# Kernel tuning notes

Measured on AMD Instinct MI355X. Metric: run time of the kernel, lower is better.

## Reference

```python
import jax, jax.numpy as jnp
import numpy as np
from jax import lax

MIN_R = 0.01
RADIUS = 0.8
NSAMPLE = 32
PRED_NSAMPLE = 16
TEMPERATURE = 1.0
DIV_COEF = 10.0
GRID3 = 64  # grid_size**3, grid_size=4
EPS = 1e-5


def _ball_query(q, xyz, radius, nsample):
    """q (M,3), xyz (N,3), radius scalar or (M,). Returns idx (M,nsample) int32, empty (M,) bool.
    Mirrors stack ball_query CUDA op: first-found neighbors within radius, padded with first index."""
    N = xyz.shape[0]
    d2 = jnp.sum((q[:, None, :] - xyz[None, :, :]) ** 2, axis=-1)  # (M,N)
    r = jnp.broadcast_to(jnp.asarray(radius, d2.dtype), (q.shape[0],))[:, None]
    valid = d2 < r * r
    score = jnp.where(valid, -jnp.arange(N, dtype=jnp.int32), -(N + 1))
    vals, _ = lax.top_k(score, nsample)  # largest score == smallest valid index
    idx = -vals
    pad = idx == (N + 1)
    idx = jnp.where(pad, idx[:, :1], idx)  # pad with first found neighbor
    empty = pad[:, 0]                       # no neighbor at all
    idx = jnp.where(empty[:, None], 0, idx)
    return idx, empty


def _group(q, xyz, feats, idx, empty):
    """QueryAndGroup gather: relative xyz concat point features; zero empty queries.
    Returns (M, nsample, 3+C)."""
    g_xyz = xyz[idx] - q[:, None, :]
    g = jnp.concatenate([g_xyz, feats[idx]], axis=-1)
    return jnp.where(empty[:, None, None], jnp.zeros((), g.dtype), g)


def _mlp(x, params):
    """Shared 1x1 Conv2d + BatchNorm2d(training stats) + ReLU stack. x: (B,M,S,C)."""
    for W, g, b in params:
        x = jnp.einsum('bmsc,cd->bmsd', x, W)
        mu = x.mean(axis=(0, 1, 2))
        var = x.var(axis=(0, 1, 2))
        x = (x - mu) * lax.rsqrt(var + EPS) * g + b
        x = jax.nn.relu(x)
    return x


def setup_inputs() -> dict:
    key = jax.random.key(0)
    ks = jax.random.split(key, 16)
    B, N, C, R, Croi = 2, 8192, 32, 64, 128
    scene = jnp.array([10.0, 10.0, 4.0], jnp.float32)
    xyz = jax.random.uniform(ks[0], (B, N, 3), jnp.float32) * scene
    features = jax.random.normal(ks[1], (B, N, C), jnp.float32)
    rois = jax.random.uniform(ks[2], (B, R, GRID3, 3), jnp.float32) * scene
    roi_features = jax.random.normal(ks[3], (B, R, Croi), jnp.float32)

    def kaiming(k, fi, fo):
        return jax.random.normal(k, (fi, fo), jnp.float32) * np.float32(np.sqrt(2.0 / fi))

    return {
        'xyz': xyz, 'features': features, 'rois': rois, 'roi_features': roi_features,
        'temperature_decay': jnp.ones((1,), jnp.float32),
        # predict mlp: [32+3, 32, 32]
        'pw0': kaiming(ks[4], 35, 32), 'pg0': jnp.ones(32), 'pb0': jnp.zeros(32),
        'pw1': kaiming(ks[5], 32, 32), 'pg1': jnp.ones(32), 'pb1': jnp.zeros(32),
        # feat mlp: [32+3, 64, 64]
        'fw0': kaiming(ks[6], 35, 64), 'fg0': jnp.ones(64), 'fb0': jnp.zeros(64),
        'fw1': kaiming(ks[7], 64, 64), 'fg1': jnp.ones(64), 'fb1': jnp.zeros(64),
        # predict fc: [32*64 + 128, 1]
        'fcw': kaiming(ks[8], 2176, 1), 'fcb': jnp.zeros(1),
    }


def reference(xyz, features, rois, roi_features, temperature_decay,
              pw0, pg0, pb0, pw1, pg1, pb1,
              fw0, fg0, fb0, fw1, fg1, fb1, fcw, fcb):
    B, num_rois = rois.shape[0], rois.shape[1]
    new_xyz = rois.reshape(B, -1, 3)  # (B, M, 3), M = num_rois*grid^3

    # ---- radius-prediction branch: fixed-radius grouping + MLP + max-pool ----
    idx_p, empty_p = jax.vmap(lambda q, x: _ball_query(q, x, RADIUS, PRED_NSAMPLE))(new_xyz, xyz)
    gp = jax.vmap(_group)(new_xyz, xyz, features, idx_p, empty_p)  # (B,M,S,3+C)
    gp = _mlp(gp, [(pw0, pg0, pb0), (pw1, pg1, pb1)])
    pooled = gp.max(axis=2)                       # (B, M, Cp)
    pooled = pooled.reshape(B, num_rois, -1)      # (B, R, grid^3*Cp)
    res = jnp.concatenate([pooled, roi_features], axis=-1) @ fcw + fcb  # (B,R,1)
    r = jnp.maximum(res / DIV_COEF + RADIUS, MIN_R)
    r_pts = jnp.broadcast_to(r, (B, num_rois, GRID3)).reshape(B, -1)    # (B, M)

    # ---- deformable branch: per-query radius grouping + soft weights ----
    idx_d, empty_d = jax.vmap(lambda q, x, rr: _ball_query(q, x, rr, NSAMPLE))(new_xyz, xyz, r_pts)
    gd = jax.vmap(_group)(new_xyz, xyz, features, idx_d, empty_d)       # (B,M,S,3+C)
    dist = jnp.linalg.norm(gd[..., :3], axis=-1)                        # (B,M,S)
    w = jax.nn.sigmoid((r_pts[..., None] - dist) / (TEMPERATURE * temperature_decay[0]))
    w = jnp.where(empty_d[..., None], jnp.zeros((), w.dtype), w)
    gd = _mlp(gd, [(fw0, fg0, fb0), (fw1, fg1, fb1)])                   # (B,M,S,Cout)
    new_feats = (w[..., None] * gd).max(axis=2)                          # (B,M,Cout)

    return new_xyz.reshape(-1, 3), new_feats.reshape(-1, new_feats.shape[-1])
```

## Files before the change

### kernel.cpp

```cpp
#include <hip/hip_runtime.h>
#include <hip/hip_fp16.h>

#define NB 2
#define NPTS 8192
#define NQ 4096
#define MTOT 8192
#define SP 16
#define SD 32
#define CIN 32
#define CP 32
#define CF 64
#define NROI 128
#define RADIUS_C 0.8f
#define MIN_R_C 0.01f
#define DIV_COEF_C 10.0f

#define INV_CS 1.25f
#define NCX 13
#define NCY 13
#define NCZ 5
#define NCELL (NCX * NCY * NCZ)

__device__ int    g_idx_p[MTOT * SP];
__device__ int    g_empty_p[MTOT];
__device__ int    g_idx_d[MTOT * SD];
__device__ int    g_empty_d[MTOT];
__device__ int    g_cellcnt[NB][NCELL];
__device__ int    g_cellcur[NB][NCELL];
__device__ int    g_cellstart[NB][NCELL + 1];
__device__ float4 g_cellxyzw[NB][NPTS];
__device__ unsigned char g_xa[(size_t)MTOT * SD * CF * 2];
__device__ unsigned char g_xb[(size_t)MTOT * SD * CF * 2];
__device__ unsigned int g_w1h[CF * CF / 2];
__device__ float  g_psT[CF * 2048];
__device__ float  g_pqT[CF * 2048];
__device__ float  g_bnscale[4][CF];
__device__ float  g_bnshift[4][CF];
__device__ float  g_rroi[NROI];

typedef _Float16 h2v __attribute__((ext_vector_type(2)));
__device__ __forceinline__ float fdot2f(unsigned int a, unsigned int b, float c) {
#if defined(__has_builtin)
#if __has_builtin(__builtin_amdgcn_fdot2)
    h2v ha, hb;
    ha = *(h2v*)&a; hb = *(h2v*)&b;
    return __builtin_amdgcn_fdot2(ha, hb, c, false);
#else
    __half2 ha = *(__half2*)&a, hb = *(__half2*)&b;
    float2 fa = __half22float2(ha), fb = __half22float2(hb);
    return fmaf(fa.x, fb.x, fmaf(fa.y, fb.y, c));
#endif
#else
    __half2 ha = *(__half2*)&a, hb = *(__half2*)&b;
    float2 fa = __half22float2(ha), fb = __half22float2(hb);
    return fmaf(fa.x, fb.x, fmaf(fa.y, fb.y, c));
#endif
}

__device__ __forceinline__ int cell_of(float x, float y, float z) {
    int cx = min(NCX - 1, max(0, (int)floorf(x * INV_CS)));
    int cy = min(NCY - 1, max(0, (int)floorf(y * INV_CS)));
    int cz = min(NCZ - 1, max(0, (int)floorf(z * INV_CS)));
    return (cz * NCY + cy) * NCX + cx;
}

#define SETUP_N (MTOT * 3 + CF * CF / 2 + NB * NCELL)
__global__ void setup_kernel(const float* __restrict__ rois, const float* __restrict__ fw1,
                             float* __restrict__ out) {
    int i = blockIdx.x * 256 + threadIdx.x;
    if (i < MTOT * 3) { out[i] = rois[i]; return; }
    i -= MTOT * 3;
    if (i < CF * CF / 2) {
        int ch = i >> 5, c2 = i & 31;
        __half2 h = __floats2half2_rn(fw1[(2 * c2) * CF + ch], fw1[(2 * c2 + 1) * CF + ch]);
        g_w1h[i] = *(unsigned int*)&h;
        return;
    }
    i -= CF * CF / 2;
    if (i < NB * NCELL) ((int*)g_cellcnt)[i] = 0;
}

__global__ void grid_count_kernel(const float* __restrict__ xyz) {
    int i = blockIdx.x * 256 + threadIdx.x;
    int b = i >> 13;
    int cell = cell_of(xyz[(size_t)i * 3 + 0], xyz[(size_t)i * 3 + 1], xyz[(size_t)i * 3 + 2]);
    atomicAdd(&g_cellcnt[b][cell], 1);
}

__global__ void grid_prefix_kernel() {
    __shared__ int sc[1024];
    int b = blockIdx.x, tid = threadIdx.x;
    int v = (tid < NCELL) ? g_cellcnt[b][tid] : 0;
    sc[tid] = v;
    __syncthreads();
    for (int off = 1; off < 1024; off <<= 1) {
        int add = (tid >= off) ? sc[tid - off] : 0;
        __syncthreads();
        sc[tid] += add;
        __syncthreads();
    }
    if (tid < NCELL) {
        int excl = sc[tid] - v;
        g_cellstart[b][tid] = excl;
        g_cellcur[b][tid] = excl;
    }
    if (tid == 0) g_cellstart[b][NCELL] = NPTS;
}

__global__ void grid_scatter_kernel(const float* __restrict__ xyz) {
    int i = blockIdx.x * 256 + threadIdx.x;
    int b = i >> 13, il = i & (NPTS - 1);
    float x = xyz[(size_t)i * 3 + 0];
    float y = xyz[(size_t)i * 3 + 1];
    float z = xyz[(size_t)i * 3 + 2];
    int cell = cell_of(x, y, z);
    int pos = atomicAdd(&g_cellcur[b][cell], 1);
    g_cellxyzw[b][pos] = make_float4(x, y, z, __int_as_float(il));
}

template <int NS>
__launch_bounds__(256, 8)
__global__ void bq_grid_kernel(const float* __restrict__ xyz, const float* __restrict__ newxyz) {
    __shared__ int s_cand[4][512];
    __shared__ int s_meta[4][2];
    int tid = threadIdx.x, wv = tid >> 6, lane = tid & 63;
    int q = blockIdx.x * 4 + wv;
    int b = q >> 12;
    float qx = newxyz[q * 3 + 0], qy = newxyz[q * 3 + 1], qz = newxyz[q * 3 + 2];
    float r = (NS == SP) ? RADIUS_C : g_rroi[q >> 6];
    float r2 = r * r;
    int* idx_out   = (NS == SP) ? g_idx_p   : g_idx_d;
    int* empty_out = (NS == SP) ? g_empty_p : g_empty_d;

    if (lane == 0) s_meta[wv][0] = 0;
    __asm__ volatile("s_waitcnt lgkmcnt(0)" ::: "memory");

    float rp = r + 1e-4f;
    int xlo = max(0, min(NCX - 1, (int)floorf((qx - rp) * INV_CS)));
    int xhi = max(0, min(NCX - 1, (int)floorf((qx + rp) * INV_CS)));
    int ylo = max(0, min(NCY - 1, (int)floorf((qy - rp) * INV_CS)));
    int yhi = max(0, min(NCY - 1, (int)floorf((qy + rp) * INV_CS)));
    int zlo = max(0, min(NCZ - 1, (int)floorf((qz - rp) * INV_CS)));
    int zhi = max(0, min(NCZ - 1, (int)floorf((qz + rp) * INV_CS)));
    int nx = xhi - xlo + 1, ny = yhi - ylo + 1, nz = zhi - zlo + 1;
    int ncell = nx * ny * nz;

    bool ovf = false;
    for (int ci = lane; ci < ncell; ci += 64) {
        int cx = xlo + (ci % nx);
        int t1 = ci / nx;
        int cy = ylo + (t1 % ny);
        int cz = zlo + (t1 / ny);
        int cell = (cz * NCY + cy) * NCX + cx;
        int s0 = g_cellstart[b][cell], e0 = g_cellstart[b][cell + 1];
        for (int e = s0; e < e0; ++e) {
            float4 v = g_cellxyzw[b][e];
            float dx = qx - v.x, dy = qy - v.y, dz = qz - v.z;
            if (dx * dx + dy * dy + dz * dz < r2) {
                int pos = atomicAdd(&s_meta[wv][0], 1);
                if (pos < 512) s_cand[wv][pos] = __float_as_int(v.w);
                else ovf = true;
            }
        }
    }
    __asm__ volatile("s_waitcnt lgkmcnt(0) vmcnt(0)" ::: "memory");
    int cnt = s_meta[wv][0];

    if (__ballot(ovf)) {
        const float* xb = xyz + (size_t)b * NPTS * 3;
        int cnt2 = 0, first_idx = 0;
        for (int g = 0; g < NPTS / 64 && cnt2 < NS; ++g) {
            int p = (g << 6) + lane;
            float dx = qx - xb[3 * p + 0];
            float dy = qy - xb[3 * p + 1];
            float dz = qz - xb[3 * p + 2];
            bool valid = (dx * dx + dy * dy + dz * dz) < r2;
            unsigned long long mask = __ballot(valid);
            if (cnt2 == 0 && mask) first_idx = (g << 6) + (int)__builtin_ctzll(mask);
            int pos = cnt2 + __popcll(mask & ((1ull << lane) - 1ull));
            if (valid && pos < NS) idx_out[q * NS + pos] = p;
            cnt2 += (int)__popcll(mask);
        }
        if (cnt2 == 0) {
            if (lane < NS) idx_out[q * NS + lane] = 0;
            if (lane == 0) empty_out[q] = 1;
        } else {
            int filled = cnt2 < NS ? cnt2 : NS;
            if (lane >= filled && lane < NS) idx_out[q * NS + lane] = first_idx;
            if (lane == 0) empty_out[q] = 0;
        }
        return;
    }

    if (cnt == 0) {
        if (lane < NS) idx_out[q * NS + lane] = 0;
        if (lane == 0) empty_out[q] = 1;
        return;
    }
    for (int i = lane; i < cnt; i += 64) {
        int c = s_cand[wv][i];
        int rank = 0;
        for (int j = 0; j < cnt; ++j) rank += (s_cand[wv][j] < c) ? 1 : 0;
        if (rank < NS) idx_out[q * NS + rank] = c;
        if (rank == 0) s_meta[wv][1] = c;
    }
    __asm__ volatile("s_waitcnt lgkmcnt(0)" ::: "memory");
    if (cnt < NS && lane >= cnt && lane < NS) idx_out[q * NS + lane] = s_meta[wv][1];
    if (lane == 0) empty_out[q] = 0;
}

template <int NS, int CH, bool HALF>
__launch_bounds__(256, 6)
__global__ void mlp_passA_kernel(const float* __restrict__ xyz, const float* __restrict__ feats,
                                 const float* __restrict__ newxyz, const float* __restrict__ W0,
                                 void* __restrict__ xout_) {
    constexpr int GSTR = 37;
    constexpr int SST  = CH + 2;
    constexpr int CHH  = CH / 2;
    __shared__ float buf[128 * GSTR];
    __shared__ float ls[256], lq[256];
    int tid = threadIdx.x;
    int row = tid & 127, half = tid >> 7;
    int halfu = __builtin_amdgcn_readfirstlane(half);
    int rowbase = blockIdx.x * 128;
    int grow = rowbase + row;
    int q = grow / NS, b = q >> 12;
    const int* idx_arr = (NS == SP) ? g_idx_p : g_idx_d;
    const int* emp_arr = (NS == SP) ? g_empty_p : g_empty_d;
    {
        float* dst = &buf[row * GSTR];
        if (emp_arr[q]) {
            int c0 = half ? 18 : 0, c1 = half ? 35 : 18;
            for (int c = c0; c < c1; ++c) dst[c] = 0.f;
        } else {
            int idx = idx_arr[grow];
            if (half == 0) {
                const float* xp = xyz + (size_t)b * NPTS * 3 + idx * 3;
                dst[0] = xp[0] - newxyz[q * 3 + 0];
                dst[1] = xp[1] - newxyz[q * 3 + 1];
                dst[2] = xp[2] - newxyz[q * 3 + 2];
            }
            const float4* fp = (const float4*)(feats + (size_t)b * NPTS * CIN + (size_t)idx * CIN);
#pragma unroll
            for (int j = 0; j < 4; ++j) {
                float4 v = fp[half * 4 + j];
                float* d = dst + 3 + (half * 4 + j) * 4;
                d[0] = v.x; d[1] = v.y; d[2] = v.z; d[3] = v.w;
            }
        }
    }
    __syncthreads();
    float acc[CHH];
#pragma unroll
    for (int ch = 0; ch < CHH; ++ch) acc[ch] = 0.f;
    {
        const float* inrow = &buf[row * GSTR];
        const float* w = W0 + halfu * CHH;
        for (int c = 0; c < 35; ++c) {
            float h = inrow[c];
#pragma unroll
            for (int ch = 0; ch < CHH; ++ch) acc[ch] = fmaf(h, w[c * CH + ch], acc[ch]);
        }
    }
    float* xf = (float*)xout_;
    __half* xh = (__half*)xout_;
    float sum = 0.f, sq = 0.f;
#pragma unroll
    for (int p = 0; p < 2; ++p) {
        __syncthreads();
        if ((row >> 6) == p) {
            float* srow = &buf[(row & 63) * SST + half * CHH];
#pragma unroll
            for (int ch = 0; ch < CHH; ++ch) srow[ch] = acc[ch];
        }
        __syncthreads();
        if (CH == 64) {
            int ch = tid & 63, rg = tid >> 6;
            for (int r = 0; r < 16; ++r) {
                float v = buf[(rg * 16 + r) * SST + ch];
                size_t o = (size_t)(rowbase + p * 64 + rg * 16 + r) * CH + ch;
                if (HALF) xh[o] = __float2half_rn(v); else xf[o] = v;
                sum += v; sq += v * v;
            }
        } else {
            int ch = tid & 31, rg = tid >> 5;
            for (int r = 0; r < 8; ++r) {
                float v = buf[(rg * 8 + r) * SST + ch];
                size_t o = (size_t)(rowbase + p * 64 + rg * 8 + r) * CH + ch;
                if (HALF) xh[o] = __float2half_rn(v); else xf[o] = v;
                sum += v; sq += v * v;
            }
        }
    }
    ls[tid] = sum; lq[tid] = sq;
    __syncthreads();
    if (CH == 64) {
        if (tid < 64) {
            g_psT[tid * 2048 + blockIdx.x] = ls[tid] + ls[64 + tid] + ls[128 + tid] + ls[192 + tid];
            g_pqT[tid * 2048 + blockIdx.x] = lq[tid] + lq[64 + tid] + lq[128 + tid] + lq[192 + tid];
        }
    } else {
        if (tid < 32) {
            float s = 0.f, qq = 0.f;
#pragma unroll
            for (int k = 0; k < 8; ++k) { s += ls[tid + 32 * k]; qq += lq[tid + 32 * k]; }
            g_psT[tid * 2048 + blockIdx.x] = s;
            g_pqT[tid * 2048 + blockIdx.x] = qq;
        }
    }
}

template <int NS, int CH>
__launch_bounds__(128, 4)
__global__ void mlp_passB_kernel(const float* __restrict__ W1, const float* __restrict__ xin,
                                 float* __restrict__ xout, int bn0) {
    constexpr int HSTR = 33;
    constexpr int SST  = CH + 2;
    __shared__ float buf[128 * 37];
    __shared__ float ls[128], lq[128];
    int tid = threadIdx.x;
    int rowbase = blockIdx.x * 128;
    const float* sc0 = g_bnscale[bn0];
    const float* sh0 = g_bnshift[bn0];
    float acc2[CH];
#pragma unroll
    for (int ch = 0; ch < CH; ++ch) acc2[ch] = 0.f;
    const float4* src = (const float4*)xin;
#pragma unroll
    for (int hc = 0; hc < CH / 32; ++hc) {
        if (hc) __syncthreads();
#pragma unroll
        for (int k = 0; k < 8; ++k) {
            int o4 = tid + k * 128;
            int rloc = o4 >> 3, j = o4 & 7;
            int c = 4 * j, gc = hc * 32 + c;
            float4 v = src[(size_t)(rowbase + rloc) * (CH / 4) + hc * 8 + j];
            float* d = &buf[rloc * HSTR + c];
            d[0] = fmaxf(fmaf(v.x, sc0[gc + 0], sh0[gc + 0]), 0.f);
            d[1] = fmaxf(fmaf(v.y, sc0[gc + 1], sh0[gc + 1]), 0.f);
            d[2] = fmaxf(fmaf(v.z, sc0[gc + 2], sh0[gc + 2]), 0.f);
            d[3] = fmaxf(fmaf(v.w, sc0[gc + 3], sh0[gc + 3]), 0.f);
        }
        __syncthreads();
        const float* hrow = &buf[tid * HSTR];
        for (int c = 0; c < 32; ++c) {
            float h = hrow[c];
#pragma unroll
            for (int ch = 0; ch < CH; ++ch)
                acc2[ch] = fmaf(h, W1[(hc * 32 + c) * CH + ch], acc2[ch]);
        }
    }
    float sum = 0.f, sq = 0.f;
#pragma unroll
    for (int p = 0; p < 2; ++p) {
        __syncthreads();
        if ((tid >> 6) == p) {
            float* srow = &buf[(tid & 63) * SST];
#pragma unroll
            for (int ch = 0; ch < CH; ++ch) srow[ch] = acc2[ch];
        }
        __syncthreads();
        int ch = tid & 31, rg = tid >> 5;
        for (int r = 0; r < 16; ++r) {
            float v = buf[(rg * 16 + r) * SST + ch];
            xout[(size_t)(rowbase + p * 64 + rg * 16 + r) * CH + ch] = v;
            sum += v; sq += v * v;
        }
    }
    ls[tid] = sum; lq[tid] = sq;
    __syncthreads();
    if (tid < 32) {
        g_psT[tid * 2048 + blockIdx.x] = ls[tid] + ls[32 + tid] + ls[64 + tid] + ls[96 + tid];
        g_pqT[tid * 2048 + blockIdx.x] = lq[tid] + lq[32 + tid] + lq[64 + tid] + lq[96 + tid];
    }
}

__launch_bounds__(256, 6)
__global__ void mlp_fB_kernel(const __half* __restrict__ xin, __half* __restrict__ xout) {
    __shared__ unsigned int hp[128 * 33];
    __shared__ float ls[256], lq[256];
    int tid = threadIdx.x;
    int row = tid & 127, half = tid >> 7;
    int halfu = __builtin_amdgcn_readfirstlane(half);
    int rowbase = blockIdx.x * 128;
    const float* sc0 = g_bnscale[2];
    const float* sh0 = g_bnshift[2];
    {
        const float4* src = (const float4*)xin;
#pragma unroll
        for (int k = 0; k < 4; ++k) {
            int o4 = tid + k * 256;
            int rloc = o4 >> 3, j = o4 & 7;
            float4 v = src[(size_t)(rowbase + rloc) * 8 + j];
            const __half2* ph = (const __half2*)&v;
            unsigned int* d = &hp[rloc * 33 + 4 * j];
#pragma unroll
            for (int m = 0; m < 4; ++m) {
                float2 f = __half22float2(ph[m]);
                int gc = 8 * j + 2 * m;
                float a = fmaxf(fmaf(f.x, sc0[gc + 0], sh0[gc + 0]), 0.f);
                float bb = fmaxf(fmaf(f.y, sc0[gc + 1], sh0[gc + 1]), 0.f);
                __half2 hh = __floats2half2_rn(a, bb);
                d[m] = *(unsigned int*)&hh;
            }
        }
    }
    __syncthreads();
    float acc[32];
#pragma unroll
    for (int ch = 0; ch < 32; ++ch) acc[ch] = 0.f;
    {
        const unsigned int* hrow = &hp[row * 33];
        const unsigned int* wbase = g_w1h + (halfu * 32) * 32;
#pragma unroll
        for (int c2 = 0; c2 < 32; ++c2) {
            unsigned int h2 = hrow[c2];
#pragma unroll
            for (int ch = 0; ch < 32; ++ch)
                acc[ch] = fdot2f(h2, wbase[ch * 32 + c2], acc[ch]);
        }
    }
    float* fview = (float*)hp;
    float sum = 0.f, sq = 0.f;
#pragma unroll
    for (int p = 0; p < 2; ++p) {
        __syncthreads();
        if ((row >> 6) == p) {
            float* srow = &fview[(row & 63) * 66 + half * 32];
#pragma unroll
            for (int ch = 0; ch < 32; ++ch) srow[ch] = acc[ch];
        }
        __syncthreads();
        int ch = tid & 63, rg = tid >> 6;
        for (int r = 0; r < 16; ++r) {
            float v = fview[(rg * 16 + r) * 66 + ch];
            xout[(size_t)(rowbase + p * 64 + rg * 16 + r) * CF + ch] = __float2half_rn(v);
            sum += v; sq += v * v;
        }
    }
    ls[tid] = sum; lq[tid] = sq;
    __syncthreads();
    if (tid < 64) {
        g_psT[tid * 2048 + blockIdx.x] = ls[tid] + ls[64 + tid] + ls[128 + tid] + ls[192 + tid];
        g_pqT[tid * 2048 + blockIdx.x] = lq[tid] + lq[64 + tid] + lq[128 + tid] + lq[192 + tid];
    }
}

__global__ void finalize_kernel(const float* __restrict__ gamma, const float* __restrict__ beta,
                                float n, int layer, int nblocks) {
    __shared__ double l_s[256], l_q[256];
    int ch = blockIdx.x, tid = threadIdx.x;
    double s = 0, q = 0;
    for (int i = tid; i < nblocks; i += 256) { s += g_psT[ch * 2048 + i]; q += g_pqT[ch * 2048 + i]; }
    l_s[tid] = s; l_q[tid] = q; __syncthreads();
    for (int off = 128; off > 0; off >>= 1) {
        if (tid < off) { l_s[tid] += l_s[tid + off]; l_q[tid] += l_q[tid + off]; }
        __syncthreads();
    }
    if (tid == 0) {
        double mu = l_s[0] / (double)n;
        double var = l_q[0] / (double)n - mu * mu;
        if (var < 0) var = 0;
        double sc = (double)gamma[ch] / sqrt(var + 1e-5);
        g_bnscale[layer][ch] = (float)sc;
        g_bnshift[layer][ch] = (float)((double)beta[ch] - mu * sc);
    }
}

__global__ void passC_f_kernel(const float* __restrict__ xyz, const float* __restrict__ newxyz,
                               const float* __restrict__ td, const __half* __restrict__ xin,
                               float* __restrict__ out) {
    __shared__ float lw[64];
    int tid = threadIdx.x;
    int qpair = blockIdx.x * 2;
    if (tid < 64) {
        int ql = tid >> 5, s = tid & 31;
        int q = qpair + ql;
        float wv = 0.f;
        if (!g_empty_d[q]) {
            int idx = g_idx_d[q * SD + s];
            int b = q >> 12;
            float dx = xyz[(size_t)b * NPTS * 3 + idx * 3 + 0] - newxyz[q * 3 + 0];
            float dy = xyz[(size_t)b * NPTS * 3 + idx * 3 + 1] - newxyz[q * 3 + 1];
            float dz = xyz[(size_t)b * NPTS * 3 + idx * 3 + 2] - newxyz[q * 3 + 2];
            float dist = sqrtf(dx * dx + dy * dy + dz * dz);
            float rq = g_rroi[q >> 6];
            wv = 1.f / (1.f + expf(-(rq - dist) / td[0]));
        }
        lw[tid] = wv;
    }
    __syncthreads();
    int ql = tid >> 6, ch = tid & 63;
    int q = qpair + ql;
    float sc = g_bnscale[3][ch], sh = g_bnshift[3][ch];
    float m = 0.f;
    for (int s = 0; s < SD; ++s) {
        float v = __half2float(xin[((size_t)q * SD + s) * CF + ch]);
        m = fmaxf(m, lw[ql * 32 + s] * fmaxf(fmaf(v, sc, sh), 0.f));
    }
    out[MTOT * 3 + (size_t)q * CF + ch] = m;
}

__global__ void passC_roi_kernel(const float* __restrict__ fcw, const float* __restrict__ fcb,
                                 const float* __restrict__ roif, const float* __restrict__ xin) {
    __shared__ float red[256];
    int tid = threadIdx.x;
    int roi = blockIdx.x;
    int ch = tid & 31, qs = tid >> 5;
    float sc = g_bnscale[1][ch], sh = g_bnshift[1][ch];
    float acc = 0.f;
    for (int ql = qs; ql < 64; ql += 8) {
        int q = roi * 64 + ql;
        float m = 0.f;
        for (int s = 0; s < SP; ++s) {
            float v = xin[(size_t)(q * SP + s) * CP + ch] * sc + sh;
            m = fmaxf(m, fmaxf(v, 0.f));
        }
        acc += m * fcw[ql * CP + ch];
    }
    if (tid < 128) acc += roif[roi * 128 + tid] * fcw[2048 + tid];
    red[tid] = acc;
    __syncthreads();
    for (int off = 128; off > 0; off >>= 1) {
        if (tid < off) red[tid] += red[tid + off];
        __syncthreads();
    }
    if (tid == 0)
        g_rroi[roi] = fmaxf((red[0] + fcb[0]) / DIV_COEF_C + RADIUS_C, MIN_R_C);
}

extern "C" void kernel_launch(void* const* d_in, const int* in_sizes, int n_in,
                              void* d_out, int out_size, void* d_ws, size_t ws_size,
                              hipStream_t stream) {
    const float* xyz   = (const float*)d_in[0];
    const float* feats = (const float*)d_in[1];
    const float* rois  = (const float*)d_in[2];
    const float* roif  = (const float*)d_in[3];
    const float* td    = (const float*)d_in[4];
    const float* pw0 = (const float*)d_in[5];
    const float* pg0 = (const float*)d_in[6];
    const float* pb0 = (const float*)d_in[7];
    const float* pw1 = (const float*)d_in[8];
    const float* pg1 = (const float*)d_in[9];
    const float* pb1 = (const float*)d_in[10];
    const float* fw0 = (const float*)d_in[11];
    const float* fg0 = (const float*)d_in[12];
    const float* fb0 = (const float*)d_in[13];
    const float* fw1 = (const float*)d_in[14];
    const float* fg1 = (const float*)d_in[15];
    const float* fb1 = (const float*)d_in[16];
    const float* fcw = (const float*)d_in[17];
    const float* fcb = (const float*)d_in[18];
    float* out = (float*)d_out;

    void* xa; hipGetSymbolAddress(&xa, HIP_SYMBOL(g_xa));
    void* xb; hipGetSymbolAddress(&xb, HIP_SYMBOL(g_xb));

    setup_kernel<<<(SETUP_N + 255) / 256, 256, 0, stream>>>(rois, fw1, out);
    grid_count_kernel<<<64, 256, 0, stream>>>(xyz);
    grid_prefix_kernel<<<2, 1024, 0, stream>>>();
    grid_scatter_kernel<<<64, 256, 0, stream>>>(xyz);

    bq_grid_kernel<SP><<<MTOT / 4, 256, 0, stream>>>(xyz, rois);
    mlp_passA_kernel<SP, CP, false><<<1024, 256, 0, stream>>>(xyz, feats, rois, pw0, xa);
    finalize_kernel<<<CP, 256, 0, stream>>>(pg0, pb0, (float)(MTOT * SP), 0, 1024);
    mlp_passB_kernel<SP, CP><<<1024, 128, 0, stream>>>(pw1, (const float*)xa, (float*)xb, 0);
    finalize_kernel<<<CP, 256, 0, stream>>>(pg1, pb1, (float)(MTOT * SP), 1, 1024);
    passC_roi_kernel<<<NROI, 256, 0, stream>>>(fcw, fcb, roif, (const float*)xb);

    bq_grid_kernel<SD><<<MTOT / 4, 256, 0, stream>>>(xyz, rois);
    mlp_passA_kernel<SD, CF, true><<<2048, 256, 0, stream>>>(xyz, feats, rois, fw0, xa);
    finalize_kernel<<<CF, 256, 0, stream>>>(fg0, fb0, (float)(MTOT * SD), 2, 2048);
    mlp_fB_kernel<<<2048, 256, 0, stream>>>((const __half*)xa, (__half*)xb);
    finalize_kernel<<<CF, 256, 0, stream>>>(fg1, fb1, (float)(MTOT * SD), 3, 2048);
    passC_f_kernel<<<MTOT / 2, 128, 0, stream>>>(xyz, rois, td, (const __half*)xb, out);
}
```

Before: 272.8 us.

## Use MFMA 16x16x32 f16 for second deformable MLP layer GEMM

Replaces the per-thread fdot2 scalar GEMM in mlp_fB_kernel with matrix-core MFMA 16x16x32 f16 instructions. Weights are preloaded into registers as fragments and A-fragments are read from padded LDS. BN partial statistics are now reduced with wave shuffles instead of an LDS transpose pass, which removes two sync rounds. Occupancy hint drops from 6 to 4 blocks, and output stores now come directly from MFMA layout, which may be less coalesced.

```diff
diff --git a/kernel.cpp b/kernel.cpp
--- a/kernel.cpp
+++ b/kernel.cpp
@@ -38,24 +38,9 @@
 __device__ float  g_bnshift[4][CF];
 __device__ float  g_rroi[NROI];
 
-typedef _Float16 h2v __attribute__((ext_vector_type(2)));
-__device__ __forceinline__ float fdot2f(unsigned int a, unsigned int b, float c) {
-#if defined(__has_builtin)
-#if __has_builtin(__builtin_amdgcn_fdot2)
-    h2v ha, hb;
-    ha = *(h2v*)&a; hb = *(h2v*)&b;
-    return __builtin_amdgcn_fdot2(ha, hb, c, false);
-#else
-    __half2 ha = *(__half2*)&a, hb = *(__half2*)&b;
-    float2 fa = __half22float2(ha), fb = __half22float2(hb);
-    return fmaf(fa.x, fb.x, fmaf(fa.y, fb.y, c));
-#endif
-#else
-    __half2 ha = *(__half2*)&a, hb = *(__half2*)&b;
-    float2 fa = __half22float2(ha), fb = __half22float2(hb);
-    return fmaf(fa.x, fb.x, fmaf(fa.y, fb.y, c));
-#endif
-}
+typedef _Float16 h2v  __attribute__((ext_vector_type(2)));
+typedef _Float16 f16x8 __attribute__((ext_vector_type(8)));
+typedef float    f32x4 __attribute__((ext_vector_type(4)));
 
 __device__ __forceinline__ int cell_of(float x, float y, float z) {
     int cx = min(NCX - 1, max(0, (int)floorf(x * INV_CS)));
@@ -375,13 +360,11 @@
     }
 }
 
-__launch_bounds__(256, 6)
+__launch_bounds__(256, 4)
 __global__ void mlp_fB_kernel(const __half* __restrict__ xin, __half* __restrict__ xout) {
-    __shared__ unsigned int hp[128 * 33];
-    __shared__ float ls[256], lq[256];
-    int tid = threadIdx.x;
-    int row = tid & 127, half = tid >> 7;
-    int halfu = __builtin_amdgcn_readfirstlane(half);
+    __shared__ __align__(16) unsigned int hp[128 * 36];
+    __shared__ float lsum[4][64], lsq[4][64];
+    int tid = threadIdx.x, wv = tid >> 6, lane = tid & 63;
     int rowbase = blockIdx.x * 128;
     const float* sc0 = g_bnscale[2];
     const float* sh0 = g_bnshift[2];
@@ -393,7 +376,7 @@
             int rloc = o4 >> 3, j = o4 & 7;
             float4 v = src[(size_t)(rowbase + rloc) * 8 + j];
             const __half2* ph = (const __half2*)&v;
-            unsigned int* d = &hp[rloc * 33 + 4 * j];
+            unsigned int* d = &hp[rloc * 36 + 4 * j];
 #pragma unroll
             for (int m = 0; m < 4; ++m) {
                 float2 f = __half22float2(ph[m]);
@@ -405,44 +388,63 @@
             }
         }
     }
-    __syncthreads();
-    float acc[32];
-#pragma unroll
-    for (int ch = 0; ch < 32; ++ch) acc[ch] = 0.f;
+    f16x8 bf[4][2];
     {
-        const unsigned int* hrow = &hp[row * 33];
-        const unsigned int* wbase = g_w1h + (halfu * 32) * 32;
-#pragma unroll
-        for (int c2 = 0; c2 < 32; ++c2) {
-            unsigned int h2 = hrow[c2];
-#pragma unroll
-            for (int ch = 0; ch < 32; ++ch)
-                acc[ch] = fdot2f(h2, wbase[ch * 32 + c2], acc[ch]);
-        }
-    }
-    float* fview = (float*)hp;
-    float sum = 0.f, sq = 0.f;
-#pragma unroll
-    for (int p = 0; p < 2; ++p) {
-        __syncthreads();
-        if ((row >> 6) == p) {
-            float* srow = &fview[(row & 63) * 66 + half * 32];
-#pragma unroll
-            for (int ch = 0; ch < 32; ++ch) srow[ch] = acc[ch];
-        }
-        __syncthreads();
-        int ch = tid & 63, rg = tid >> 6;
-        for (int r = 0; r < 16; ++r) {
-            float v = fview[(rg * 16 + r) * 66 + ch];
-            xout[(size_t)(rowbase + p * 64 + rg * 16 + r) * CF + ch] = __float2half_rn(v);
-            sum += v; sq += v * v;
-        }
-    }
-    ls[tid] = sum; lq[tid] = sq;
+        int chl = lane & 15, kg = lane >> 4;
+#pragma unroll
+        for (int ct = 0; ct < 4; ++ct)
+#pragma unroll
+            for (int kt = 0; kt < 2; ++kt)
+                bf[ct][kt] = *(const f16x8*)(g_w1h + (ct * 16 + chl) * 32 + kt * 16 + kg * 4);
+    }
+    __syncthreads();
+    f32x4 acc[2][4];
+#pragma unroll
+    for (int rt = 0; rt < 2; ++rt)
+#pragma unroll
+        for (int ct = 0; ct < 4; ++ct) acc[rt][ct] = (f32x4){0.f, 0.f, 0.f, 0.f};
+#pragma unroll
+    for (int rt = 0; rt < 2; ++rt) {
+        int row = wv * 32 + rt * 16 + (lane & 15);
+#pragma unroll
+        for (int kt = 0; kt < 2; ++kt) {
+            f16x8 a = *(const f16x8*)&hp[row * 36 + kt * 16 + (lane >> 4) * 4];
+#pragma unroll
+            for (int ct = 0; ct < 4; ++ct)
+                acc[rt][ct] = __builtin_amdgcn_mfma_f32_16x16x32_f16(a, bf[ct][kt], acc[rt][ct], 0, 0, 0);
+        }
+    }
+    float s[4] = {0.f, 0.f, 0.f, 0.f}, q[4] = {0.f, 0.f, 0.f, 0.f};
+#pragma unroll
+    for (int rt = 0; rt < 2; ++rt) {
+        int rbase = rowbase + wv * 32 + rt * 16 + (lane >> 4) * 4;
+#pragma unroll
+        for (int ct = 0; ct < 4; ++ct) {
+            int ch = ct * 16 + (lane & 15);
+#pragma unroll
+            for (int i = 0; i < 4; ++i) {
+                float v = acc[rt][ct][i];
+                xout[(size_t)(rbase + i) * CF + ch] = __float2half_rn(v);
+                s[ct] += v; q[ct] += v * v;
+            }
+        }
+    }
+#pragma unroll
+    for (int ct = 0; ct < 4; ++ct) {
+        s[ct] += __shfl_xor(s[ct], 16, 64); s[ct] += __shfl_xor(s[ct], 32, 64);
+        q[ct] += __shfl_xor(q[ct], 16, 64); q[ct] += __shfl_xor(q[ct], 32, 64);
+    }
+    if (lane < 16) {
+#pragma unroll
+        for (int ct = 0; ct < 4; ++ct) {
+            lsum[wv][ct * 16 + lane] = s[ct];
+            lsq[wv][ct * 16 + lane] = q[ct];
+        }
+    }
     __syncthreads();
     if (tid < 64) {
-        g_psT[tid * 2048 + blockIdx.x] = ls[tid] + ls[64 + tid] + ls[128 + tid] + ls[192 + tid];
-        g_pqT[tid * 2048 + blockIdx.x] = lq[tid] + lq[64 + tid] + lq[128 + tid] + lq[192 + tid];
+        g_psT[tid * 2048 + blockIdx.x] = lsum[0][tid] + lsum[1][tid] + lsum[2][tid] + lsum[3][tid];
+        g_pqT[tid * 2048 + blockIdx.x] = lsq[0][tid] + lsq[1][tid] + lsq[2][tid] + lsq[3][tid];
     }
 }
 
```

New measurement: 252.6 us (median of 2 runs). -7.4%, faster.
